# Optimization experiments

Hardware: AMD Instinct MI355X
Metric: run time of the kernel (lower is better)

Reference implementation:

```python
import jax, jax.numpy as jnp
import numpy as np

B = 1      # batch
D = 64     # octree grid side at this level
N = 65536  # active voxels
C = 32     # channels (nin == nout for resblock)
K = 3      # kernel size


def _offsets():
    r = jnp.arange(K) - K // 2
    oz, oy, ox = jnp.meshgrid(r, r, r, indexing='ij')
    return jnp.stack([oz.ravel(), oy.ravel(), ox.ravel()], axis=-1)  # [27,3] (kz,ky,kx order)


def octree_conv3d(values, indices, mask_values, kernel, bias, activation=None):
    # values: [N,Cin], indices: [N,4] (b,z,y,x), mask_values: [N,1]
    Cin = values.shape[-1]
    Cout = kernel.shape[-1]
    taps = kernel.reshape(K * K * K, Cin, Cout)            # kz,ky,kx order == kernel[kz,ky,kx]
    vals = jnp.einsum('nc,tcd->tnd', values, taps)         # [27,N,Cout]
    offs = _offsets()                                      # [27,3]
    coords = indices[:, 1:]                                # [N,3]
    # shift = [0, kz-1, ky-1, kx-1]; clamp to [0, D-1] (stride=inv_stride=1)
    sh = jnp.clip(coords[None, :, :] + offs[:, None, :], 0, D - 1)  # [27,N,3]
    lin = indices[:, 0][None, :] * (D * D * D) + sh[..., 0] * (D * D) + sh[..., 1] * D + sh[..., 2]
    grid = jnp.zeros((B * D * D * D, Cout), dtype=values.dtype)
    grid = grid.at[lin.reshape(-1)].add(vals.reshape(-1, Cout))     # scatter-add == coalesce sum
    out_lin = indices[:, 0] * (D * D * D) + coords[:, 0] * (D * D) + coords[:, 1] * D + coords[:, 2]
    gathered = grid[out_lin]                               # [N,Cout] values at mask positions
    out = (gathered + mask_values * bias[None, :]) * mask_values     # result + mask*bias; result*mask
    if activation is not None:
        out = activation(out)
    return out


def setup_inputs() -> dict:
    key = jax.random.key(0)
    k1, k2, k3, k4, k5, k6 = jax.random.split(key, 6)
    G = B * D * D * D
    perm = jax.random.permutation(k1, G)[:N]               # unique (coalesced) voxel indices
    b = perm // (D * D * D)
    rem = perm % (D * D * D)
    z = rem // (D * D)
    y = (rem // D) % D
    x = rem % D
    indices = jnp.stack([b, z, y, x], axis=-1).astype(jnp.int64)   # [N,4]
    values = jax.random.normal(k2, (N, C), dtype=jnp.float32)
    mask_values = jnp.ones((N, 1), dtype=jnp.float32)
    stdv = 1.0 / np.sqrt(K * K * K * C)
    kern1 = (jax.random.uniform(k3, (K, K, K, C, C)) - 0.5) * 2.0 * stdv
    bias1 = (jax.random.uniform(k4, (C,)) - 0.5) * 2.0 * stdv
    kern2 = (jax.random.uniform(k5, (K, K, K, C, C)) - 0.5) * 2.0 * stdv
    bias2 = (jax.random.uniform(k6, (C,)) - 0.5) * 2.0 * stdv
    return {'values': values, 'indices': indices, 'mask_values': mask_values,
            'kern1': kern1, 'bias1': bias1, 'kern2': kern2, 'bias2': bias2}


def reference(values, indices, mask_values, kern1, bias1, kern2, bias2):
    # OctreeResblock: conv(relu) -> conv -> residual add, all on the sparse index set
    h = octree_conv3d(values, indices, mask_values, kern1, bias1, activation=jax.nn.relu)
    h = octree_conv3d(h, indices, mask_values, kern2, bias2, activation=None)
    return values + h
```

## Files before the change

kernel.cpp:

```cpp
#include <hip/hip_runtime.h>

#define NPTS 65536
#define CCH  32
#define DDIM 64
#define GVOX (DDIM*DDIM*DDIM)
#define MAXTILES 4128

typedef _Float16 half8  __attribute__((ext_vector_type(8)));
typedef _Float16 half4v __attribute__((ext_vector_type(4)));
typedef float    floatx4 __attribute__((ext_vector_type(4)));

__global__ __launch_bounds__(256) void k_prep0(
    int* __restrict__ map, int* __restrict__ sorted,
    const float* __restrict__ values, _Float16* __restrict__ valsh,
    const float* __restrict__ k1, const float* __restrict__ k2,
    _Float16* __restrict__ w1, _Float16* __restrict__ w2,
    _Float16* __restrict__ hh, int* __restrict__ pcoord,
    int* __restrict__ cnt, int* __restrict__ slot)
{
  int tid = blockIdx.x * 256 + threadIdx.x;
  if (tid < GVOX/4) { ((int4*)map)[tid] = make_int4(-1,-1,-1,-1); return; }
  tid -= GVOX/4;
  if (tid < MAXTILES*16) { sorted[tid] = NPTS; return; }
  tid -= MAXTILES*16;
  if (tid < (NPTS*CCH)/4) {
    float4 v = ((const float4*)values)[tid];
    half4v h = { (_Float16)v.x, (_Float16)v.y, (_Float16)v.z, (_Float16)v.w };
    ((half4v*)valsh)[tid] = h; return;
  }
  tid -= (NPTS*CCH)/4;
  if (tid < 27*CCH*CCH) {
    int t = tid/(CCH*CCH), r = tid%(CCH*CCH);
    int cin = r/CCH, cout = r%CCH;
    int o = (t*CCH + cout)*CCH + cin;
    w1[o] = (_Float16)k1[tid]; w2[o] = (_Float16)k2[tid]; return;
  }
  tid -= 27*CCH*CCH;
  if (tid < CCH) { valsh[NPTS*CCH+tid] = (_Float16)0.f; hh[NPTS*CCH+tid] = (_Float16)0.f; return; }
  tid -= CCH;
  if (tid < 27) { cnt[tid] = 0; slot[tid] = 0; return; }
  tid -= 27;
  if (tid == 0) pcoord[NPTS] = 0;
}
#define PREP0_THREADS (GVOX/4 + MAXTILES*16 + (NPTS*CCH)/4 + 27*CCH*CCH + CCH + 27 + 1)

__global__ __launch_bounds__(256) void k_prep1(const int* __restrict__ idx,
                                               int* __restrict__ map,
                                               int* __restrict__ pcoord,
                                               int* __restrict__ cls,
                                               int* __restrict__ cnt)
{
  __shared__ int lcnt[27];
  if (threadIdx.x < 27) lcnt[threadIdx.x] = 0;
  __syncthreads();
  const int n = blockIdx.x*256 + threadIdx.x;
  const int b = idx[4*n], z = idx[4*n+1], y = idx[4*n+2], x = idx[4*n+3];
  map[((b*DDIM + z)*DDIM + y)*DDIM + x] = n;
  pcoord[n] = (b<<18) | (z<<12) | (y<<6) | x;
  const int cz = (z==0)?0:((z==DDIM-1)?2:1);
  const int cy = (y==0)?0:((y==DDIM-1)?2:1);
  const int cx = (x==0)?0:((x==DDIM-1)?2:1);
  const int c = cz*9 + cy*3 + cx;
  cls[n] = c;
  atomicAdd(&lcnt[c], 1);
  __syncthreads();
  if (threadIdx.x < 27 && lcnt[threadIdx.x]) atomicAdd(&cnt[threadIdx.x], lcnt[threadIdx.x]);
}

__global__ void k_prep2(const int* __restrict__ cnt, int* __restrict__ clsbase,
                        int* __restrict__ tstart, int* __restrict__ ntiles)
{
  if (threadIdx.x == 0 && blockIdx.x == 0) {
    int b = 0, tb = 0;
    for (int c = 0; c < 27; ++c) {
      clsbase[c] = b; tstart[c] = tb;
      int nt = (cnt[c] + 15) >> 4;
      b += nt << 4; tb += nt;
    }
    tstart[27] = tb; *ntiles = tb;
  }
}

__global__ __launch_bounds__(256) void k_prep3(const int* __restrict__ cls,
                                               const int* __restrict__ clsbase,
                                               int* __restrict__ slot,
                                               int* __restrict__ sorted,
                                               const int* __restrict__ tstart,
                                               const int* __restrict__ ntp,
                                               int* __restrict__ tileclass)
{
  if (blockIdx.x < NPTS/256) {
    __shared__ int lcnt[27], lbase[27];
    if (threadIdx.x < 27) lcnt[threadIdx.x] = 0;
    __syncthreads();
    const int n = blockIdx.x*256 + threadIdx.x;
    const int c = cls[n];
    const int lrank = atomicAdd(&lcnt[c], 1);
    __syncthreads();
    if (threadIdx.x < 27)
      lbase[threadIdx.x] = lcnt[threadIdx.x] ? atomicAdd(&slot[threadIdx.x], lcnt[threadIdx.x]) : 0;
    __syncthreads();
    sorted[clsbase[c] + lbase[c] + lrank] = n;
  } else {
    const int i = (blockIdx.x - NPTS/256)*256 + threadIdx.x;
    if (i >= MAXTILES) return;
    const int nt = *ntp;
    int c = 13;
    if (i < nt) {
      for (int cc = 0; cc < 27; ++cc)
        if (i >= tstart[cc] && i < tstart[cc+1]) { c = cc; break; }
    }
    tileclass[i] = c;
  }
}

template<int MODE>
__global__ __launch_bounds__(256) void conv_mfma(
    const _Float16* __restrict__ A,
    const int* __restrict__ map,
    const int* __restrict__ pcoord,
    const int* __restrict__ sorted,
    const int* __restrict__ tileclass,
    const int* __restrict__ ntp,
    const _Float16* __restrict__ WT,
    const float* __restrict__ bias,
    const float* __restrict__ mask,
    const float* __restrict__ resid,
    _Float16* __restrict__ hout,
    float* __restrict__ fout)
{
  const int tile = blockIdx.x*4 + (threadIdx.x >> 6);
  if (tile >= *ntp) return;
  const int lane = threadIdx.x & 63;
  const int m = lane & 15, quad = lane >> 4;
  const int scls = __builtin_amdgcn_readfirstlane(tileclass[tile]);
  const int cz = scls/9, cy = (scls/3)%3, cx = scls%3;

  const int pid = sorted[tile*16 + m];
  const int pc  = pcoord[pid];
  const int bb = pc>>18, z = (pc>>12)&63, y = (pc>>6)&63, x = pc&63;
  const int linb = bb << 18;
  const int az[3] = { max(z-1,0)<<12, z<<12, min(z+1,DDIM-1)<<12 };
  const int ay[3] = { max(y-1,0)<<6,  y<<6,  min(y+1,DDIM-1)<<6 };
  const int ax[3] = { max(x-1,0),     x,     min(x+1,DDIM-1) };

  floatx4 acc0 = {0.f,0.f,0.f,0.f};
  floatx4 acc1 = {0.f,0.f,0.f,0.f};

#pragma unroll
  for (int j = 0; j < 27; ++j) {
    const int jz = j/9, jy = (j/3)%3, jx = j%3;
    const int tz = (cz==1) ? (2-jz) : ((jz==1) ? 1 : ((cz==0) ? 0 : 2));
    const int ty = (cy==1) ? (2-jy) : ((jy==1) ? 1 : ((cy==0) ? 0 : 2));
    const int tx = (cx==1) ? (2-jx) : ((jx==1) ? 1 : ((cx==0) ? 0 : 2));
    const int t  = tz*9 + ty*3 + tx;
    int src = map[linb | az[jz] | ay[jy] | ax[jx]];
    src = (src < 0) ? NPTS : src;
    half8 a  = *(const half8*)(A + src*CCH + quad*8);
    const _Float16* wr = WT + t*(CCH*CCH);
    half8 b0 = *(const half8*)(wr + m*CCH + quad*8);
    half8 b1 = *(const half8*)(wr + (16+m)*CCH + quad*8);
    acc0 = __builtin_amdgcn_mfma_f32_16x16x32_f16(a, b0, acc0, 0, 0, 0);
    acc1 = __builtin_amdgcn_mfma_f32_16x16x32_f16(a, b1, acc1, 0, 0, 0);
  }

  const float bi0 = bias[m], bi1 = bias[m+16];
#pragma unroll
  for (int reg = 0; reg < 4; ++reg) {
    const int r  = quad*4 + reg;
    const int pr = sorted[tile*16 + r];
    if (pr >= NPTS) continue;
    const float mk = mask[pr];
    float v0 = (acc0[reg] + mk*bi0) * mk;
    float v1 = (acc1[reg] + mk*bi1) * mk;
    if (MODE == 0) {
      v0 = fmaxf(v0, 0.f); v1 = fmaxf(v1, 0.f);
      hout[pr*CCH + m]      = (_Float16)v0;
      hout[pr*CCH + m + 16] = (_Float16)v1;
    } else {
      fout[pr*CCH + m]      = resid[pr*CCH + m]      + v0;
      fout[pr*CCH + m + 16] = resid[pr*CCH + m + 16] + v1;
    }
  }
}


extern "C" void kernel_launch(void* const* d_in, const int* in_sizes, int n_in,
                              void* d_out, int out_size, void* d_ws, size_t ws_size,
                              hipStream_t stream) {
  const float* values = (const float*)d_in[0];
  const int*   indices= (const int*)  d_in[1];
  const float* maskv  = (const float*)d_in[2];
  const float* kern1  = (const float*)d_in[3];
  const float* bias1  = (const float*)d_in[4];
  const float* kern2  = (const float*)d_in[5];
  const float* bias2  = (const float*)d_in[6];
  float* out = (float*)d_out;

  char* ws = (char*)d_ws;
  size_t off = 0;
  auto alloc = [&](size_t bytes) { void* p = ws + off; off = (off + bytes + 255) & ~(size_t)255; return p; };
  int*      map      = (int*)     alloc(GVOX*4);
  int*      pcoord   = (int*)     alloc((NPTS+1)*4);
  int*      cls      = (int*)     alloc(NPTS*4);
  int*      sorted   = (int*)     alloc(MAXTILES*16*4);
  int*      tileclass= (int*)     alloc(MAXTILES*4);
  int*      cnt      = (int*)     alloc(27*4);
  int*      slot     = (int*)     alloc(27*4);
  int*      clsbase  = (int*)     alloc(27*4);
  int*      tstart   = (int*)     alloc(28*4);
  int*      ntiles   = (int*)     alloc(4);
  _Float16* valsh    = (_Float16*)alloc((NPTS+1)*CCH*2);
  _Float16* hh       = (_Float16*)alloc((NPTS+1)*CCH*2);
  _Float16* wt1      = (_Float16*)alloc(27*CCH*CCH*2);
  _Float16* wt2      = (_Float16*)alloc(27*CCH*CCH*2);

  k_prep0<<<(PREP0_THREADS + 255)/256, 256, 0, stream>>>(
      map, sorted, values, valsh, kern1, kern2, wt1, wt2, hh, pcoord, cnt, slot);
  k_prep1<<<NPTS/256, 256, 0, stream>>>(indices, map, pcoord, cls, cnt);
  k_prep2<<<1, 64, 0, stream>>>(cnt, clsbase, tstart, ntiles);
  k_prep3<<<NPTS/256 + (MAXTILES+255)/256, 256, 0, stream>>>(
      cls, clsbase, slot, sorted, tstart, ntiles, tileclass);

  conv_mfma<0><<<MAXTILES/4, 256, 0, stream>>>(valsh, map, pcoord, sorted, tileclass,
                                               ntiles, wt1, bias1, maskv, nullptr, hh, nullptr);
  conv_mfma<1><<<MAXTILES/4, 256, 0, stream>>>(hh, map, pcoord, sorted, tileclass,
                                               ntiles, wt2, bias2, maskv, values, nullptr, out);
}
```

Before: 149.7 us.

## Split conv taps across two waves per tile and fold prep2 into prep3

```diff
diff --git a/kernel.cpp b/kernel.cpp
--- a/kernel.cpp
+++ b/kernel.cpp
@@ -54,7 +54,8 @@
   if (threadIdx.x < 27) lcnt[threadIdx.x] = 0;
   __syncthreads();
   const int n = blockIdx.x*256 + threadIdx.x;
-  const int b = idx[4*n], z = idx[4*n+1], y = idx[4*n+2], x = idx[4*n+3];
+  const int4 v = ((const int4*)idx)[n];
+  const int b = v.x, z = v.y, y = v.z, x = v.w;
   map[((b*DDIM + z)*DDIM + y)*DDIM + x] = n;
   pcoord[n] = (b<<18) | (z<<12) | (y<<6) | x;
   const int cz = (z==0)?0:((z==DDIM-1)?2:1);
@@ -67,28 +68,28 @@
   if (threadIdx.x < 27 && lcnt[threadIdx.x]) atomicAdd(&cnt[threadIdx.x], lcnt[threadIdx.x]);
 }
 
-__global__ void k_prep2(const int* __restrict__ cnt, int* __restrict__ clsbase,
-                        int* __restrict__ tstart, int* __restrict__ ntiles)
-{
-  if (threadIdx.x == 0 && blockIdx.x == 0) {
-    int b = 0, tb = 0;
-    for (int c = 0; c < 27; ++c) {
-      clsbase[c] = b; tstart[c] = tb;
-      int nt = (cnt[c] + 15) >> 4;
-      b += nt << 4; tb += nt;
-    }
-    tstart[27] = tb; *ntiles = tb;
-  }
-}
-
 __global__ __launch_bounds__(256) void k_prep3(const int* __restrict__ cls,
-                                               const int* __restrict__ clsbase,
+                                               const int* __restrict__ cnt,
                                                int* __restrict__ slot,
                                                int* __restrict__ sorted,
-                                               const int* __restrict__ tstart,
-                                               const int* __restrict__ ntp,
-                                               int* __restrict__ tileclass)
-{
+                                               int* __restrict__ tileclass,
+                                               int* __restrict__ ntiles)
+{
+  __shared__ int s_clsbase[27];
+  __shared__ int s_tstart[28];
+  if (threadIdx.x == 0) {
+    int b = 0, tb = 0;
+#pragma unroll
+    for (int c = 0; c < 27; ++c) {
+      s_clsbase[c] = b; s_tstart[c] = tb;
+      const int ntc = (cnt[c] + 15) >> 4;
+      b += ntc << 4; tb += ntc;
+    }
+    s_tstart[27] = tb;
+    if (blockIdx.x == 0) *ntiles = tb;
+  }
+  __syncthreads();
+
   if (blockIdx.x < NPTS/256) {
     __shared__ int lcnt[27], lbase[27];
     if (threadIdx.x < 27) lcnt[threadIdx.x] = 0;
@@ -100,17 +101,48 @@
     if (threadIdx.x < 27)
       lbase[threadIdx.x] = lcnt[threadIdx.x] ? atomicAdd(&slot[threadIdx.x], lcnt[threadIdx.x]) : 0;
     __syncthreads();
-    sorted[clsbase[c] + lbase[c] + lrank] = n;
+    sorted[s_clsbase[c] + lbase[c] + lrank] = n;
   } else {
     const int i = (blockIdx.x - NPTS/256)*256 + threadIdx.x;
     if (i >= MAXTILES) return;
-    const int nt = *ntp;
+    const int nt = s_tstart[27];
     int c = 13;
     if (i < nt) {
       for (int cc = 0; cc < 27; ++cc)
-        if (i >= tstart[cc] && i < tstart[cc+1]) { c = cc; break; }
+        if (i >= s_tstart[cc] && i < s_tstart[cc+1]) { c = cc; break; }
     }
     tileclass[i] = c;
+  }
+}
+
+template<int J0, int J1>
+__device__ __forceinline__ void accum_taps(
+    const _Float16* __restrict__ A, const int* __restrict__ map,
+    const _Float16* __restrict__ WT,
+    int cz, int cy, int cx, int linb,
+    const int* az, const int* ay, const int* ax,
+    int m, int quad, floatx4& acc0, floatx4& acc1)
+{
+  int srcs[J1 - J0];
+#pragma unroll
+  for (int j = J0; j < J1; ++j) {
+    const int jz = j/9, jy = (j/3)%3, jx = j%3;
+    const int s = map[linb | az[jz] | ay[jy] | ax[jx]];
+    srcs[j - J0] = (s < 0) ? (NPTS*CCH) : (s*CCH);
+  }
+#pragma unroll
+  for (int j = J0; j < J1; ++j) {
+    const int jz = j/9, jy = (j/3)%3, jx = j%3;
+    const int tz = (cz==1) ? (2-jz) : ((jz==1) ? 1 : ((cz==0) ? 0 : 2));
+    const int ty = (cy==1) ? (2-jy) : ((jy==1) ? 1 : ((cy==0) ? 0 : 2));
+    const int tx = (cx==1) ? (2-jx) : ((jx==1) ? 1 : ((cx==0) ? 0 : 2));
+    const int t  = tz*9 + ty*3 + tx;
+    half8 a  = *(const half8*)(A + srcs[j - J0] + quad*8);
+    const _Float16* wr = WT + t*(CCH*CCH);
+    half8 b0 = *(const half8*)(wr + m*CCH + quad*8);
+    half8 b1 = *(const half8*)(wr + (16+m)*CCH + quad*8);
+    acc0 = __builtin_amdgcn_mfma_f32_16x16x32_f16(a, b0, acc0, 0, 0, 0);
+    acc1 = __builtin_amdgcn_mfma_f32_16x16x32_f16(a, b1, acc1, 0, 0, 0);
   }
 }
 
@@ -129,57 +161,66 @@
     _Float16* __restrict__ hout,
     float* __restrict__ fout)
 {
-  const int tile = blockIdx.x*4 + (threadIdx.x >> 6);
-  if (tile >= *ntp) return;
+  __shared__ float red[2][16][33];
+  const int wv   = threadIdx.x >> 6;
+  const int tl   = wv >> 1;
+  const int half = wv & 1;
+  const int tile = blockIdx.x*2 + tl;
+  const int nt   = *ntp;
+  const bool active = tile < nt;
   const int lane = threadIdx.x & 63;
   const int m = lane & 15, quad = lane >> 4;
-  const int scls = __builtin_amdgcn_readfirstlane(tileclass[tile]);
-  const int cz = scls/9, cy = (scls/3)%3, cx = scls%3;
-
-  const int pid = sorted[tile*16 + m];
-  const int pc  = pcoord[pid];
-  const int bb = pc>>18, z = (pc>>12)&63, y = (pc>>6)&63, x = pc&63;
-  const int linb = bb << 18;
-  const int az[3] = { max(z-1,0)<<12, z<<12, min(z+1,DDIM-1)<<12 };
-  const int ay[3] = { max(y-1,0)<<6,  y<<6,  min(y+1,DDIM-1)<<6 };
-  const int ax[3] = { max(x-1,0),     x,     min(x+1,DDIM-1) };
 
   floatx4 acc0 = {0.f,0.f,0.f,0.f};
   floatx4 acc1 = {0.f,0.f,0.f,0.f};
 
-#pragma unroll
-  for (int j = 0; j < 27; ++j) {
-    const int jz = j/9, jy = (j/3)%3, jx = j%3;
-    const int tz = (cz==1) ? (2-jz) : ((jz==1) ? 1 : ((cz==0) ? 0 : 2));
-    const int ty = (cy==1) ? (2-jy) : ((jy==1) ? 1 : ((cy==0) ? 0 : 2));
-    const int tx = (cx==1) ? (2-jx) : ((jx==1) ? 1 : ((cx==0) ? 0 : 2));
-    const int t  = tz*9 + ty*3 + tx;
-    int src = map[linb | az[jz] | ay[jy] | ax[jx]];
-    src = (src < 0) ? NPTS : src;
-    half8 a  = *(const half8*)(A + src*CCH + quad*8);
-    const _Float16* wr = WT + t*(CCH*CCH);
-    half8 b0 = *(const half8*)(wr + m*CCH + quad*8);
-    half8 b1 = *(const half8*)(wr + (16+m)*CCH + quad*8);
-    acc0 = __builtin_amdgcn_mfma_f32_16x16x32_f16(a, b0, acc0, 0, 0, 0);
-    acc1 = __builtin_amdgcn_mfma_f32_16x16x32_f16(a, b1, acc1, 0, 0, 0);
-  }
-
-  const float bi0 = bias[m], bi1 = bias[m+16];
-#pragma unroll
-  for (int reg = 0; reg < 4; ++reg) {
-    const int r  = quad*4 + reg;
-    const int pr = sorted[tile*16 + r];
-    if (pr >= NPTS) continue;
-    const float mk = mask[pr];
-    float v0 = (acc0[reg] + mk*bi0) * mk;
-    float v1 = (acc1[reg] + mk*bi1) * mk;
-    if (MODE == 0) {
-      v0 = fmaxf(v0, 0.f); v1 = fmaxf(v1, 0.f);
-      hout[pr*CCH + m]      = (_Float16)v0;
-      hout[pr*CCH + m + 16] = (_Float16)v1;
-    } else {
-      fout[pr*CCH + m]      = resid[pr*CCH + m]      + v0;
-      fout[pr*CCH + m + 16] = resid[pr*CCH + m + 16] + v1;
+  if (active) {
+    const int scls = __builtin_amdgcn_readfirstlane(tileclass[tile]);
+    const int cz = scls/9, cy = (scls/3)%3, cx = scls%3;
+    const int pid = sorted[tile*16 + m];
+    const int pc  = pcoord[pid];
+    const int bb = pc>>18, z = (pc>>12)&63, y = (pc>>6)&63, x = pc&63;
+    const int linb = bb << 18;
+    const int az[3] = { max(z-1,0)<<12, z<<12, min(z+1,DDIM-1)<<12 };
+    const int ay[3] = { max(y-1,0)<<6,  y<<6,  min(y+1,DDIM-1)<<6 };
+    const int ax[3] = { max(x-1,0),     x,     min(x+1,DDIM-1) };
+    if (half == 0)
+      accum_taps<0,14>(A, map, WT, cz,cy,cx, linb, az,ay,ax, m,quad, acc0,acc1);
+    else
+      accum_taps<14,27>(A, map, WT, cz,cy,cx, linb, az,ay,ax, m,quad, acc0,acc1);
+  }
+
+  if (active && half == 0) {
+#pragma unroll
+    for (int r = 0; r < 4; ++r) {
+      red[tl][quad*4+r][m]    = acc0[r];
+      red[tl][quad*4+r][m+16] = acc1[r];
+    }
+  }
+  __syncthreads();
+  if (active && half == 1) {
+#pragma unroll
+    for (int r = 0; r < 4; ++r) {
+      acc0[r] += red[tl][quad*4+r][m];
+      acc1[r] += red[tl][quad*4+r][m+16];
+    }
+    const float bi0 = bias[m], bi1 = bias[m+16];
+#pragma unroll
+    for (int reg = 0; reg < 4; ++reg) {
+      const int r  = quad*4 + reg;
+      const int pr = sorted[tile*16 + r];
+      if (pr >= NPTS) continue;
+      const float mk = mask[pr];
+      float v0 = (acc0[reg] + mk*bi0) * mk;
+      float v1 = (acc1[reg] + mk*bi1) * mk;
+      if (MODE == 0) {
+        v0 = fmaxf(v0, 0.f); v1 = fmaxf(v1, 0.f);
+        hout[pr*CCH + m]      = (_Float16)v0;
+        hout[pr*CCH + m + 16] = (_Float16)v1;
+      } else {
+        fout[pr*CCH + m]      = resid[pr*CCH + m]      + v0;
+        fout[pr*CCH + m + 16] = resid[pr*CCH + m + 16] + v1;
+      }
     }
   }
 }
@@ -207,8 +248,6 @@
   int*      tileclass= (int*)     alloc(MAXTILES*4);
   int*      cnt      = (int*)     alloc(27*4);
   int*      slot     = (int*)     alloc(27*4);
-  int*      clsbase  = (int*)     alloc(27*4);
-  int*      tstart   = (int*)     alloc(28*4);
   int*      ntiles   = (int*)     alloc(4);
   _Float16* valsh    = (_Float16*)alloc((NPTS+1)*CCH*2);
   _Float16* hh       = (_Float16*)alloc((NPTS+1)*CCH*2);
@@ -218,12 +257,11 @@
   k_prep0<<<(PREP0_THREADS + 255)/256, 256, 0, stream>>>(
       map, sorted, values, valsh, kern1, kern2, wt1, wt2, hh, pcoord, cnt, slot);
   k_prep1<<<NPTS/256, 256, 0, stream>>>(indices, map, pcoord, cls, cnt);
-  k_prep2<<<1, 64, 0, stream>>>(cnt, clsbase, tstart, ntiles);
   k_prep3<<<NPTS/256 + (MAXTILES+255)/256, 256, 0, stream>>>(
-      cls, clsbase, slot, sorted, tstart, ntiles, tileclass);
-
-  conv_mfma<0><<<MAXTILES/4, 256, 0, stream>>>(valsh, map, pcoord, sorted, tileclass,
+      cls, cnt, slot, sorted, tileclass, ntiles);
+
+  conv_mfma<0><<<MAXTILES/2, 256, 0, stream>>>(valsh, map, pcoord, sorted, tileclass,
                                                ntiles, wt1, bias1, maskv, nullptr, hh, nullptr);
-  conv_mfma<1><<<MAXTILES/4, 256, 0, stream>>>(hh, map, pcoord, sorted, tileclass,
+  conv_mfma<1><<<MAXTILES/2, 256, 0, stream>>>(hh, map, pcoord, sorted, tileclass,
                                                ntiles, wt2, bias2, maskv, values, nullptr, out);
 }
```

Result: faster. 145.1 us (-3.1%).
